# Performance work log

Measured on AMD Instinct MI355X. Metric: run time of the kernel, lower is better.

Reference implementation:

```python
import jax, jax.numpy as jnp
import numpy as np

HEADS = 24
HEAD_DIM = 128
DIM = HEADS * HEAD_DIM  # 3072
EPS = 1e-6


def setup_inputs() -> dict:
    key = jax.random.key(0)
    ks = jax.random.split(key, 10)
    B, S_IMG, S_TXT = 1, 2048, 256
    hidden_states = jax.random.normal(ks[0], (B, S_IMG, DIM), jnp.float32)
    encoder_hidden_states = jax.random.normal(ks[1], (B, S_TXT, DIM), jnp.float32)
    # RoPE tables for image tokens, interleaved pair layout [S_IMG, HEAD_DIM]
    inv = 1.0 / (10000.0 ** (np.arange(0, HEAD_DIM, 2, dtype=np.float32) / HEAD_DIM))
    ang = np.arange(S_IMG, dtype=np.float32)[:, None] * inv[None, :]  # [S, Dh/2]
    ang = np.repeat(ang, 2, axis=-1)  # [S, Dh], pairs (2i, 2i+1) share angle
    rope_cos = jnp.asarray(np.cos(ang), jnp.float32)
    rope_sin = jnp.asarray(np.sin(ang), jnp.float32)
    s = 0.02
    wq = jax.random.normal(ks[2], (DIM, DIM), jnp.float32) * s
    wk = jax.random.normal(ks[3], (DIM, DIM), jnp.float32) * s
    wv = jax.random.normal(ks[4], (DIM, DIM), jnp.float32) * s
    wo = jax.random.normal(ks[5], (DIM, DIM), jnp.float32) * s
    bq = jax.random.normal(ks[6], (DIM,), jnp.float32) * s
    bk = jax.random.normal(ks[7], (DIM,), jnp.float32) * s
    bv = jax.random.normal(ks[8], (DIM,), jnp.float32) * s
    bo = jax.random.normal(ks[9], (DIM,), jnp.float32) * s
    norm_q_w = jnp.ones((HEAD_DIM,), jnp.float32)
    norm_k_w = jnp.ones((HEAD_DIM,), jnp.float32)
    return dict(hidden_states=hidden_states, encoder_hidden_states=encoder_hidden_states,
                rope_cos=rope_cos, rope_sin=rope_sin,
                wq=wq, bq=bq, wk=wk, bk=bk, wv=wv, bv=bv,
                norm_q_w=norm_q_w, norm_k_w=norm_k_w, wo=wo, bo=bo)


def _rmsnorm(x, w):
    var = jnp.mean(jnp.square(x), axis=-1, keepdims=True)
    return x * jax.lax.rsqrt(var + EPS) * w


def _rope(x, cos, sin):
    # x [B,H,S,Dh]; diffusers apply_rotary_emb with use_real_unbind_dim=-1:
    # pairs are interleaved (x[2i], x[2i+1]) -> rotated = stack(-imag, real)
    xr = x[..., 0::2]
    xi = x[..., 1::2]
    x_rot = jnp.stack([-xi, xr], axis=-1).reshape(x.shape)
    return x * cos + x_rot * sin


def reference(hidden_states, encoder_hidden_states, rope_cos, rope_sin,
              wq, bq, wk, bk, wv, bv, norm_q_w, norm_k_w, wo, bo):
    B, s_img, D = hidden_states.shape
    s_txt = encoder_hidden_states.shape[1]
    S = s_img + s_txt
    x = jnp.concatenate([hidden_states, encoder_hidden_states], axis=1)  # [B,S,D]

    def proj(w, b):
        return (x @ w + b).reshape(B, S, HEADS, HEAD_DIM).transpose(0, 2, 1, 3)  # [B,H,S,Dh]

    q = _rmsnorm(proj(wq, bq), norm_q_w)
    k = _rmsnorm(proj(wk, bk), norm_k_w)
    v = proj(wv, bv)
    # RoPE on image tokens only
    q = jnp.concatenate([_rope(q[:, :, :s_img], rope_cos, rope_sin), q[:, :, s_img:]], axis=2)
    k = jnp.concatenate([_rope(k[:, :, :s_img], rope_cos, rope_sin), k[:, :, s_img:]], axis=2)
    scale = 1.0 / jnp.sqrt(jnp.float32(HEAD_DIM))
    scores = jnp.einsum('bhqd,bhkd->bhqk', q, k) * scale
    attn = jax.nn.softmax(scores, axis=-1)
    out = jnp.einsum('bhqk,bhkd->bhqd', attn, v)
    out = out.transpose(0, 2, 1, 3).reshape(B, S, D)
    img = out[:, :s_img] @ wo + bo  # to_out[0]; to_out[1] is Dropout(p=0) -> identity
    txt = out[:, s_img:]            # to_add_out is None in this branch
    return img, txt
```

## Files before the change

kernel.cpp:

```cpp
#include <hip/hip_runtime.h>
#include <cstdint>

typedef __bf16 bf16_t;
typedef bf16_t bf16x8 __attribute__((ext_vector_type(8)));
typedef bf16_t bf16x4 __attribute__((ext_vector_type(4)));
typedef float  floatx4 __attribute__((ext_vector_type(4)));

#define S_ALL 2304
#define SIMG  2048
#define NH    24
#define HD    128
#define DIM   3072
#define NQKV  9216

#define SHIFT2 17.312340490667562f
#define QSCALE 0.12751744f

typedef __attribute__((address_space(1))) void* gp1_t;
typedef __attribute__((address_space(3))) void* lp3_t;

__device__ __forceinline__ void async16(const void* g, void* l) {
    __builtin_amdgcn_global_load_lds((gp1_t)(g), (lp3_t)(l), 16, 0, 0);
}
__device__ __forceinline__ floatx4 mfma_bf16(bf16x8 a, bf16x8 b, floatx4 c) {
    return __builtin_amdgcn_mfma_f32_16x16x32_bf16(a, b, c, 0, 0, 0);
}
__device__ __forceinline__ void barrier_raw() {
    asm volatile("s_barrier" ::: "memory");
}

__global__ __launch_bounds__(256) void k_convert_x(const float* __restrict__ hid,
                                                   const float* __restrict__ enc,
                                                   bf16_t* __restrict__ xb) {
    long i = ((long)blockIdx.x * 256 + threadIdx.x) * 4;
    const long HN = (long)SIMG * DIM;
    float4 f = (i < HN) ? *(const float4*)(hid + i) : *(const float4*)(enc + (i - HN));
    bf16x4 o;
    o[0] = (bf16_t)f.x; o[1] = (bf16_t)f.y; o[2] = (bf16_t)f.z; o[3] = (bf16_t)f.w;
    *(bf16x4*)(xb + i) = o;
}

__global__ __launch_bounds__(256) void k_wT4(const float* __restrict__ wq, const float* __restrict__ wk,
                                             const float* __restrict__ wv, const float* __restrict__ wo,
                                             bf16_t* __restrict__ wTq, bf16_t* __restrict__ woT) {
    __shared__ __align__(16) bf16_t T[64][72];
    int z = blockIdx.z;
    const float* W = (z == 0) ? wq : (z == 1) ? wk : (z == 2) ? wv : wo;
    bf16_t* Wt = (z < 3) ? (wTq + (long)z * DIM * DIM) : woT;
    int r0 = blockIdx.x * 64, c0 = blockIdx.y * 64;
    int tid = threadIdx.x;
    int lr = tid >> 2, lc = (tid & 3) * 16;
    const float* src = W + (long)(r0 + lr) * DIM + c0 + lc;
#pragma unroll
    for (int i = 0; i < 16; i += 4) {
        float4 f = *(const float4*)(src + i);
        T[lr][lc + i + 0] = (bf16_t)f.x;
        T[lr][lc + i + 1] = (bf16_t)f.y;
        T[lr][lc + i + 2] = (bf16_t)f.z;
        T[lr][lc + i + 3] = (bf16_t)f.w;
    }
    __syncthreads();
    bf16x8 a, b;
#pragma unroll
    for (int i = 0; i < 8; i++) a[i] = T[lc + i][lr];
#pragma unroll
    for (int i = 0; i < 8; i++) b[i] = T[lc + 8 + i][lr];
    bf16_t* dst = Wt + (long)(c0 + lr) * DIM + r0 + lc;
    *(bf16x8*)dst = a;
    *(bf16x8*)(dst + 8) = b;
}

__device__ __forceinline__ void gemm_pipe_256x128(const bf16_t* __restrict__ A,
                                                  const bf16_t* __restrict__ Bt,
                                                  long m0, long n0, const int K,
                                                  char* smem, int tid,
                                                  floatx4 acc[4][4]) {
    const int wave = tid >> 6, lane = tid & 63;
    const int quad = lane >> 4, l16 = lane & 15;
    const int wm = (wave >> 1) * 64;
    const int wn = (wave & 1) * 64;
    const int kxor = ((lane & 7) ^ ((lane >> 3) & 7)) * 8;
    const bf16_t* Ag = A + (m0 + wave * 32 + (lane >> 3)) * K + kxor;
    const bf16_t* Bg = Bt + (n0 + wave * 16 + (lane >> 3)) * K + kxor;
    char* Asl = smem + wave * 4096;
    char* Bsl = smem + 98304 + wave * 2048;

    const int NT = K >> 6;

#pragma unroll
    for (int c2 = 0; c2 < 4; ++c2) async16(Ag + (long)c2 * 8 * K,      Asl + c2 * 1024);
#pragma unroll
    for (int c2 = 0; c2 < 2; ++c2) async16(Bg + (long)c2 * 8 * K,      Bsl + c2 * 1024);
#pragma unroll
    for (int c2 = 0; c2 < 4; ++c2) async16(Ag + (long)c2 * 8 * K + 64, Asl + 32768 + c2 * 1024);
#pragma unroll
    for (int c2 = 0; c2 < 2; ++c2) async16(Bg + (long)c2 * 8 * K + 64, Bsl + 16384 + c2 * 1024);
    asm volatile("s_waitcnt vmcnt(6)" ::: "memory");
    barrier_raw();

    int cur = 0;
    for (int kt = 0; kt < NT; ++kt) {
        const bf16_t* As = (const bf16_t*)(smem + cur * 32768);
        const bf16_t* Bs = (const bf16_t*)(smem + 98304 + cur * 16384);
        int nxt = cur + 2; if (nxt >= 3) nxt -= 3;
        char* Asd = Asl + nxt * 32768;
        char* Bsd = Bsl + nxt * 16384;
        const long kg = (long)(kt + 2) * 64;
        const bool issue = (kt < NT - 2);

        bf16x8 af[4], bfr[4];
        {
            int ch = (quad ^ (l16 & 7)) * 8;
#pragma unroll
            for (int i = 0; i < 4; i++) af[i]  = *(const bf16x8*)&As[(wm + i * 16 + l16) * 64 + ch];
#pragma unroll
            for (int j = 0; j < 4; j++) bfr[j] = *(const bf16x8*)&Bs[(wn + j * 16 + l16) * 64 + ch];
        }
        if (issue) {
            async16(Ag + kg,          Asd);
            async16(Ag + 8 * K + kg,  Asd + 1024);
            async16(Bg + kg,          Bsd);
        }
        barrier_raw();
        __builtin_amdgcn_s_setprio(1);
#pragma unroll
        for (int i = 0; i < 4; i++)
#pragma unroll
            for (int j = 0; j < 4; j++) acc[i][j] = mfma_bf16(af[i], bfr[j], acc[i][j]);
        __builtin_amdgcn_s_setprio(0);

        {
            int ch = ((4 + quad) ^ (l16 & 7)) * 8;
#pragma unroll
            for (int i = 0; i < 4; i++) af[i]  = *(const bf16x8*)&As[(wm + i * 16 + l16) * 64 + ch];
#pragma unroll
            for (int j = 0; j < 4; j++) bfr[j] = *(const bf16x8*)&Bs[(wn + j * 16 + l16) * 64 + ch];
        }
        if (issue) {
            async16(Ag + 16 * K + kg, Asd + 2048);
            async16(Ag + 24 * K + kg, Asd + 3072);
            async16(Bg + 8 * K + kg,  Bsd + 1024);
        }
        barrier_raw();
        __builtin_amdgcn_s_setprio(1);
#pragma unroll
        for (int i = 0; i < 4; i++)
#pragma unroll
            for (int j = 0; j < 4; j++) acc[i][j] = mfma_bf16(af[i], bfr[j], acc[i][j]);
        __builtin_amdgcn_s_setprio(0);

        if (issue) asm volatile("s_waitcnt vmcnt(6)" ::: "memory");
        else       asm volatile("s_waitcnt vmcnt(0)" ::: "memory");
        barrier_raw();
        cur += 1; if (cur >= 3) cur -= 3;
    }
}

__global__ __launch_bounds__(512, 2) void k_gemm_qkv(const bf16_t* __restrict__ A,
                                                     const bf16_t* __restrict__ Bt,
                                                     const float* __restrict__ bq_,
                                                     const float* __restrict__ bk_,
                                                     const float* __restrict__ bv_,
                                                     const float* __restrict__ rope_cos,
                                                     const float* __restrict__ rope_sin,
                                                     const float* __restrict__ nqw,
                                                     const float* __restrict__ nkw,
                                                     bf16_t* __restrict__ qo,
                                                     bf16_t* __restrict__ ko,
                                                     bf16_t* __restrict__ vT) {
    __shared__ __align__(16) char smem[147456];
    int tid = threadIdx.x;
    int wave = tid >> 6, lane = tid & 63;
    int quad = lane >> 4, l16 = lane & 15;
    long m0 = (long)blockIdx.y * 256, n0 = (long)blockIdx.x * 128;
    int t = blockIdx.x / 24, h = blockIdx.x % 24;
    int wm = (wave >> 1) * 64, wn = (wave & 1) * 64;

    floatx4 zero = {0.f, 0.f, 0.f, 0.f};
    floatx4 acc[4][4];
#pragma unroll
    for (int i = 0; i < 4; i++)
#pragma unroll
        for (int j = 0; j < 4; j++) acc[i][j] = zero;

    gemm_pipe_256x128(A, Bt, m0, n0, DIM, smem, tid, acc);

    int dcol[4];
#pragma unroll
    for (int j = 0; j < 4; j++) dcol[j] = wn + j * 16 + l16;

    if (t == 2) {
        float bias4[4];
#pragma unroll
        for (int j = 0; j < 4; j++) bias4[j] = bv_[h * HD + dcol[j]];
        char* vbuf = smem;
        int wmi = wave >> 1;
#pragma unroll
        for (int half = 0; half < 2; ++half) {
            if ((wmi >> 1) == half) {
#pragma unroll
                for (int i = 0; i < 4; i++)
#pragma unroll
                    for (int r = 0; r < 4; r++) {
                        int s_l = wm - half * 128 + i * 16 + quad * 4 + r;
#pragma unroll
                        for (int j = 0; j < 4; j++) {
                            int d = dcol[j];
                            int chunk = d * 16 + ((s_l >> 3) ^ (d & 15));
                            *(bf16_t*)(vbuf + chunk * 16 + (s_l & 7) * 2) = (bf16_t)(acc[i][j][r] + bias4[j]);
                        }
                    }
            }
            __syncthreads();
            int d = tid >> 2, sh = tid & 3;
            bf16_t* dstv = vT + (long)h * HD * S_ALL + (long)d * S_ALL + m0 + half * 128 + sh * 32;
#pragma unroll
            for (int k8 = 0; k8 < 4; ++k8) {
                int s8 = sh * 4 + k8;
                bf16x8 frag = *(const bf16x8*)(vbuf + (d * 16 + (s8 ^ (d & 15))) * 16);
                *(bf16x8*)(dstv + k8 * 8) = frag;
            }
            __syncthreads();
        }
    } else {
        float* ssq = (float*)smem;
        const float* bp = t ? bk_ : bq_;
        const float* nw = t ? nkw : nqw;
        float bias4[4], wv4[4];
#pragma unroll
        for (int j = 0; j < 4; j++) {
            bias4[j] = bp[h * HD + dcol[j]];
            wv4[j] = nw[dcol[j]];
        }
        int wnh = wave & 1;
#pragma unroll
        for (int i = 0; i < 4; i++)
#pragma unroll
            for (int r = 0; r < 4; r++) {
                int row = wm + i * 16 + quad * 4 + r;
                float s2 = 0.f;
#pragma unroll
                for (int j = 0; j < 4; j++) {
                    float v = acc[i][j][r] + bias4[j];
                    acc[i][j][r] = v;
                    s2 += v * v;
                }
                s2 += __shfl_xor(s2, 1);
                s2 += __shfl_xor(s2, 2);
                s2 += __shfl_xor(s2, 4);
                s2 += __shfl_xor(s2, 8);
                if (l16 == 0) ssq[row * 2 + wnh] = s2;
            }
        __syncthreads();
        bf16_t* dst = (t ? ko : qo) + (long)h * S_ALL * HD;
        bool do_rope = (m0 < SIMG);
#pragma unroll
        for (int i = 0; i < 4; i++)
#pragma unroll
            for (int r = 0; r < 4; r++) {
                int row = wm + i * 16 + quad * 4 + r;
                int s_abs = (int)m0 + row;
                float tot = ssq[row * 2] + ssq[row * 2 + 1];
                float rms = rsqrtf(tot * (1.0f / 128.0f) + 1e-6f);
                float y[4];
#pragma unroll
                for (int j = 0; j < 4; j++) y[j] = acc[i][j][r] * rms * wv4[j];
                if (do_rope) {
                    const float* cp = rope_cos + (long)s_abs * HD;
                    const float* sp = rope_sin + (long)s_abs * HD;
#pragma unroll
                    for (int j = 0; j < 4; j++) {
                        float c = cp[dcol[j]], sn = sp[dcol[j]];
                        float px = __shfl_xor(y[j], 1);
                        y[j] = y[j] * c + ((l16 & 1) ? px : -px) * sn;
                    }
                }
#pragma unroll
                for (int j = 0; j < 4; j++) {
                    float v = t ? y[j] : y[j] * QSCALE;
                    dst[(long)s_abs * HD + dcol[j]] = (bf16_t)v;
                }
            }
    }
}

__global__ __launch_bounds__(512, 2) void k_gemm_bt(const bf16_t* __restrict__ A,
                                                    const bf16_t* __restrict__ Bt,
                                                    const float* __restrict__ bias,
                                                    bf16_t* __restrict__ Cb, float* __restrict__ Cf,
                                                    int M, int N, int K) {
    __shared__ __align__(16) char smem[147456];
    int tid = threadIdx.x;
    int wave = tid >> 6, lane = tid & 63;
    int quad = lane >> 4, l16 = lane & 15;
    long m0 = (long)blockIdx.y * 256, n0 = (long)blockIdx.x * 128;
    int wm = (wave >> 1) * 64, wn = (wave & 1) * 64;

    floatx4 zero = {0.f, 0.f, 0.f, 0.f};
    floatx4 acc[4][4];
#pragma unroll
    for (int i = 0; i < 4; i++)
#pragma unroll
        for (int j = 0; j < 4; j++) acc[i][j] = zero;

    gemm_pipe_256x128(A, Bt, m0, n0, K, smem, tid, acc);

#pragma unroll
    for (int i = 0; i < 4; i++) {
        long rowb = m0 + wm + i * 16 + quad * 4;
#pragma unroll
        for (int j = 0; j < 4; j++) {
            long col = n0 + wn + j * 16 + l16;
            float bv = bias ? bias[col] : 0.0f;
#pragma unroll
            for (int r = 0; r < 4; r++) {
                float v = acc[i][j][r] + bv;
                long idx = (rowb + r) * N + col;
                if (Cb) Cb[idx] = (bf16_t)v;
                else    Cf[idx] = v;
            }
        }
    }
}

__global__ __launch_bounds__(256, 2) void k_attn(const bf16_t* __restrict__ q,
                                                 const bf16_t* __restrict__ k,
                                                 const bf16_t* __restrict__ vT,
                                                 bf16_t* __restrict__ ao,
                                                 float* __restrict__ out_txt) {
    __shared__ __align__(16) bf16_t Ks[64 * 128];
    __shared__ __align__(16) bf16_t VTs[128 * 64];
    __shared__ __align__(16) bf16_t Ps[4][2][16 * 64];
    int tid = threadIdx.x, wave = tid >> 6, lane = tid & 63;
    int quad = lane >> 4, l16 = lane & 15;
    int h = blockIdx.y;
    int q0 = blockIdx.x * 128 + wave * 32;
    const long hbase = (long)h * S_ALL * HD;
    const char* kgb = (const char*)(k + hbase);
    const char* vgb = (const char*)(vT + hbase);

    int koffB[4], voffB[4], slotB[4];
#pragma unroll
    for (int c2 = 0; c2 < 4; ++c2) {
        int L = (wave * 4 + c2) * 64 + lane;
        slotB[c2] = L;
        int rk = L >> 4, ck = (L & 15) ^ (rk & 15);
        koffB[c2] = rk * 256 + ck * 16;
        int rv = L >> 3, cv = (L & 7) ^ (rv & 7) ^ (((rv >> 3) & 1) << 2);
        voffB[c2] = rv * (S_ALL * 2) + cv * 16;
    }

    bf16x8 qf[2][4];
#pragma unroll
    for (int st = 0; st < 2; ++st) {
        const bf16_t* qp = q + hbase + (long)(q0 + st * 16 + l16) * HD + quad * 8;
#pragma unroll
        for (int ks = 0; ks < 4; ++ks) qf[st][ks] = *(const bf16x8*)(qp + ks * 32);
    }

    floatx4 zero = {0.f, 0.f, 0.f, 0.f};
    floatx4 o0[8], o1[8];
#pragma unroll
    for (int ni = 0; ni < 8; ++ni) { o0[ni] = zero; o1[ni] = zero; }
    floatx4 lac0 = zero, lac1 = zero;

    for (int kb = 0; kb < S_ALL / 64; ++kb) {
        const char* kg = kgb + (long)kb * 16384;
        const char* vg = vgb + kb * 128;
#pragma unroll
        for (int c2 = 0; c2 < 4; ++c2) {
            async16(kg + koffB[c2], (char*)Ks + slotB[c2] * 16);
            async16(vg + voffB[c2], (char*)VTs + slotB[c2] * 16);
        }
        __syncthreads();

        floatx4 s0[4], s1[4];
#pragma unroll
        for (int ni = 0; ni < 4; ++ni) { s0[ni] = zero; s1[ni] = zero; }
#pragma unroll
        for (int ks = 0; ks < 4; ++ks)
#pragma unroll
            for (int ni = 0; ni < 4; ++ni) {
                int slot = (ni * 16 + l16) * 16 + ((ks * 4 + quad) ^ l16);
                bf16x8 kf = *(const bf16x8*)&Ks[slot * 8];
                s0[ni] = mfma_bf16(qf[0][ks], kf, s0[ni]);
                s1[ni] = mfma_bf16(qf[1][ks], kf, s1[ni]);
            }

#pragma unroll
        for (int st = 0; st < 2; ++st) {
#pragma unroll
            for (int ni = 0; ni < 4; ++ni) {
                floatx4 sv = st ? s1[ni] : s0[ni];
                floatx4 p;
#pragma unroll
                for (int j = 0; j < 4; ++j) p[j] = __builtin_amdgcn_exp2f(sv[j] - SHIFT2);
                if (st) lac1 += p; else lac0 += p;
#pragma unroll
                for (int j = 0; j < 4; ++j) {
                    int r = quad * 4 + j;
                    int chunk = ((ni * 16 + l16) >> 3) ^ ((r >> 1) & 7);
                    Ps[wave][st][r * 64 + chunk * 8 + (l16 & 7)] = (bf16_t)p[j];
                }
            }
        }

        bf16x8 pf[2][2];
#pragma unroll
        for (int st = 0; st < 2; ++st)
#pragma unroll
            for (int k2 = 0; k2 < 2; ++k2) {
                int chunk = (k2 * 4 + quad) ^ ((l16 >> 1) & 7);
                pf[st][k2] = *(const bf16x8*)&Ps[wave][st][l16 * 64 + chunk * 8];
            }

#pragma unroll
        for (int k2 = 0; k2 < 2; ++k2)
#pragma unroll
            for (int ni = 0; ni < 8; ++ni) {
                int r = ni * 16 + l16;
                int c = (k2 * 4 + quad) ^ (l16 & 7) ^ (((l16 >> 3) & 1) << 2);
                bf16x8 vf = *(const bf16x8*)&VTs[r * 64 + c * 8];
                o0[ni] = mfma_bf16(pf[0][k2], vf, o0[ni]);
                o1[ni] = mfma_bf16(pf[1][k2], vf, o1[ni]);
            }
        __syncthreads();
    }

#pragma unroll
    for (int off = 1; off < 16; off <<= 1) {
#pragma unroll
        for (int j = 0; j < 4; ++j) {
            lac0[j] += __shfl_xor(lac0[j], off);
            lac1[j] += __shfl_xor(lac1[j], off);
        }
    }

#pragma unroll
    for (int st = 0; st < 2; ++st) {
#pragma unroll
        for (int j = 0; j < 4; ++j) {
            float rl = 1.0f / (st ? lac1[j] : lac0[j]);
            int s_row = q0 + st * 16 + quad * 4 + j;
#pragma unroll
            for (int ni = 0; ni < 8; ++ni) {
                float v = (st ? o1[ni][j] : o0[ni][j]) * rl;
                int col = h * HD + ni * 16 + l16;
                ao[(long)s_row * DIM + col] = (bf16_t)v;
                if (s_row >= SIMG) out_txt[(long)(s_row - SIMG) * DIM + col] = v;
            }
        }
    }
}

extern "C" void kernel_launch(void* const* d_in, const int* in_sizes, int n_in,
                              void* d_out, int out_size, void* d_ws, size_t ws_size,
                              hipStream_t stream) {
    const float* hid = (const float*)d_in[0];
    const float* enc = (const float*)d_in[1];
    const float* rope_cos = (const float*)d_in[2];
    const float* rope_sin = (const float*)d_in[3];
    const float* wq = (const float*)d_in[4];
    const float* bq = (const float*)d_in[5];
    const float* wk = (const float*)d_in[6];
    const float* bk = (const float*)d_in[7];
    const float* wv = (const float*)d_in[8];
    const float* bv = (const float*)d_in[9];
    const float* nqw = (const float*)d_in[10];
    const float* nkw = (const float*)d_in[11];
    const float* wo = (const float*)d_in[12];
    const float* bo = (const float*)d_in[13];
    float* out = (float*)d_out;

    char* ws = (char*)d_ws;
    bf16_t* xb   = (bf16_t*)(ws);
    bf16_t* wTq  = (bf16_t*)(ws + 14155776L);
    bf16_t* woT  = (bf16_t*)(ws + 70778880L);
    bf16_t* qb   = (bf16_t*)(ws + 89653248L);
    bf16_t* kbuf = (bf16_t*)(ws + 103809024L);
    bf16_t* vT   = (bf16_t*)(ws + 117964800L);
    bf16_t* ao   = (bf16_t*)(ws + 132120576L);

    k_convert_x<<<6912, 256, 0, stream>>>(hid, enc, xb);
    k_wT4<<<dim3(48, 48, 4), 256, 0, stream>>>(wq, wk, wv, wo, wTq, woT);
    k_gemm_qkv<<<dim3(72, 9), 512, 0, stream>>>(xb, wTq, bq, bk, bv, rope_cos, rope_sin,
                                                nqw, nkw, qb, kbuf, vT);
    k_attn<<<dim3(18, 24), 256, 0, stream>>>(qb, kbuf, vT, ao, out + (long)SIMG * DIM);
    k_gemm_bt<<<dim3(24, 8), 512, 0, stream>>>(ao, woT, bo, (bf16_t*)nullptr, out, SIMG, DIM, DIM);
}
```

Baseline: 519.4 us.

## Merge GEMM K-halves into one barrier phase and swizzle block order for XCDs

The GEMM main loop now issues all six async global-to-LDS loads up front, reads both K-halves of the A/B fragments from LDS at once, and runs all 32 MFMAs between a single pair of barriers instead of two. This removes one barrier per K-tile at the cost of holding twice the fragment registers. Both GEMM kernels also switch to a 1-D grid with a block-index swizzle ((bid&7)*stride + bid>>3). The swizzle is meant to group neighbouring tiles on the same XCD so they share L2.

```diff
diff --git a/kernel.cpp b/kernel.cpp
--- a/kernel.cpp
+++ b/kernel.cpp
@@ -108,45 +108,38 @@
         const long kg = (long)(kt + 2) * 64;
         const bool issue = (kt < NT - 2);
 
-        bf16x8 af[4], bfr[4];
-        {
-            int ch = (quad ^ (l16 & 7)) * 8;
-#pragma unroll
-            for (int i = 0; i < 4; i++) af[i]  = *(const bf16x8*)&As[(wm + i * 16 + l16) * 64 + ch];
-#pragma unroll
-            for (int j = 0; j < 4; j++) bfr[j] = *(const bf16x8*)&Bs[(wn + j * 16 + l16) * 64 + ch];
-        }
         if (issue) {
             async16(Ag + kg,          Asd);
             async16(Ag + 8 * K + kg,  Asd + 1024);
-            async16(Bg + kg,          Bsd);
-        }
-        barrier_raw();
-        __builtin_amdgcn_s_setprio(1);
-#pragma unroll
-        for (int i = 0; i < 4; i++)
-#pragma unroll
-            for (int j = 0; j < 4; j++) acc[i][j] = mfma_bf16(af[i], bfr[j], acc[i][j]);
-        __builtin_amdgcn_s_setprio(0);
-
-        {
-            int ch = ((4 + quad) ^ (l16 & 7)) * 8;
-#pragma unroll
-            for (int i = 0; i < 4; i++) af[i]  = *(const bf16x8*)&As[(wm + i * 16 + l16) * 64 + ch];
-#pragma unroll
-            for (int j = 0; j < 4; j++) bfr[j] = *(const bf16x8*)&Bs[(wn + j * 16 + l16) * 64 + ch];
-        }
-        if (issue) {
             async16(Ag + 16 * K + kg, Asd + 2048);
             async16(Ag + 24 * K + kg, Asd + 3072);
+            async16(Bg + kg,          Bsd);
             async16(Bg + 8 * K + kg,  Bsd + 1024);
         }
-        barrier_raw();
+
+        bf16x8 af0[4], bf0[4], af1[4], bf1[4];
+        {
+            int ch0 = (quad ^ (l16 & 7)) * 8;
+            int ch1 = ((4 + quad) ^ (l16 & 7)) * 8;
+#pragma unroll
+            for (int i = 0; i < 4; i++) af0[i] = *(const bf16x8*)&As[(wm + i * 16 + l16) * 64 + ch0];
+#pragma unroll
+            for (int j = 0; j < 4; j++) bf0[j] = *(const bf16x8*)&Bs[(wn + j * 16 + l16) * 64 + ch0];
+#pragma unroll
+            for (int i = 0; i < 4; i++) af1[i] = *(const bf16x8*)&As[(wm + i * 16 + l16) * 64 + ch1];
+#pragma unroll
+            for (int j = 0; j < 4; j++) bf1[j] = *(const bf16x8*)&Bs[(wn + j * 16 + l16) * 64 + ch1];
+        }
+
         __builtin_amdgcn_s_setprio(1);
 #pragma unroll
         for (int i = 0; i < 4; i++)
 #pragma unroll
-            for (int j = 0; j < 4; j++) acc[i][j] = mfma_bf16(af[i], bfr[j], acc[i][j]);
+            for (int j = 0; j < 4; j++) acc[i][j] = mfma_bf16(af0[i], bf0[j], acc[i][j]);
+#pragma unroll
+        for (int i = 0; i < 4; i++)
+#pragma unroll
+            for (int j = 0; j < 4; j++) acc[i][j] = mfma_bf16(af1[i], bf1[j], acc[i][j]);
         __builtin_amdgcn_s_setprio(0);
 
         if (issue) asm volatile("s_waitcnt vmcnt(6)" ::: "memory");
@@ -172,8 +165,11 @@
     int tid = threadIdx.x;
     int wave = tid >> 6, lane = tid & 63;
     int quad = lane >> 4, l16 = lane & 15;
-    long m0 = (long)blockIdx.y * 256, n0 = (long)blockIdx.x * 128;
-    int t = blockIdx.x / 24, h = blockIdx.x % 24;
+    int bid = blockIdx.x;
+    int swz = (bid & 7) * 81 + (bid >> 3);
+    int x_n = swz % 72, y_m = swz / 72;
+    long m0 = (long)y_m * 256, n0 = (long)x_n * 128;
+    int t = x_n / 24, h = x_n % 24;
     int wm = (wave >> 1) * 64, wn = (wave & 1) * 64;
 
     floatx4 zero = {0.f, 0.f, 0.f, 0.f};
@@ -293,7 +289,10 @@
     int tid = threadIdx.x;
     int wave = tid >> 6, lane = tid & 63;
     int quad = lane >> 4, l16 = lane & 15;
-    long m0 = (long)blockIdx.y * 256, n0 = (long)blockIdx.x * 128;
+    int bid = blockIdx.x;
+    int swz = (bid & 7) * 24 + (bid >> 3);
+    int x_n = swz % 24, y_m = swz / 24;
+    long m0 = (long)y_m * 256, n0 = (long)x_n * 128;
     int wm = (wave >> 1) * 64, wn = (wave & 1) * 64;
 
     floatx4 zero = {0.f, 0.f, 0.f, 0.f};
@@ -483,8 +482,8 @@
 
     k_convert_x<<<6912, 256, 0, stream>>>(hid, enc, xb);
     k_wT4<<<dim3(48, 48, 4), 256, 0, stream>>>(wq, wk, wv, wo, wTq, woT);
-    k_gemm_qkv<<<dim3(72, 9), 512, 0, stream>>>(xb, wTq, bq, bk, bv, rope_cos, rope_sin,
-                                                nqw, nkw, qb, kbuf, vT);
+    k_gemm_qkv<<<648, 512, 0, stream>>>(xb, wTq, bq, bk, bv, rope_cos, rope_sin,
+                                        nqw, nkw, qb, kbuf, vT);
     k_attn<<<dim3(18, 24), 256, 0, stream>>>(qb, kbuf, vT, ao, out + (long)SIMG * DIM);
-    k_gemm_bt<<<dim3(24, 8), 512, 0, stream>>>(ao, woT, bo, (bf16_t*)nullptr, out, SIMG, DIM, DIM);
-}
+    k_gemm_bt<<<192, 512, 0, stream>>>(ao, woT, bo, (bf16_t*)nullptr, out, SIMG, DIM, DIM);
+}
```

Result: slower. 543.4 us (+4.6%).

## Enlarge GEMM tiles to 256x256 with double-buffered pipeline

Applied to the files above, without the earlier changes.

Switches the QKV and output GEMMs from 256x128 tiles with a three-stage async LDS pipeline to 256x256 tiles with a two-stage double buffer. Each wave now holds an 8x4 accumulator block, and the QKV epilogue is reworked so one block covers two heads. The bigger tiles are meant to raise operand reuse per LDS load and halve the number of blocks. In exchange, register pressure rises, the grid shrinks (324 and 96 blocks), and the shallower prefetch with a full vmcnt(0) wait each step may expose more load latency.

```diff
diff --git a/kernel.cpp b/kernel.cpp
--- a/kernel.cpp
+++ b/kernel.cpp
@@ -70,89 +70,69 @@
     *(bf16x8*)(dst + 8) = b;
 }
 
-__device__ __forceinline__ void gemm_pipe_256x128(const bf16_t* __restrict__ A,
+__device__ __forceinline__ void gemm_pipe_256x256(const bf16_t* __restrict__ A,
                                                   const bf16_t* __restrict__ Bt,
                                                   long m0, long n0, const int K,
                                                   char* smem, int tid,
-                                                  floatx4 acc[4][4]) {
+                                                  floatx4 acc[8][4]) {
     const int wave = tid >> 6, lane = tid & 63;
     const int quad = lane >> 4, l16 = lane & 15;
-    const int wm = (wave >> 1) * 64;
-    const int wn = (wave & 1) * 64;
+    const int wm = (wave >> 2) * 128;
+    const int wn = (wave & 3) * 64;
     const int kxor = ((lane & 7) ^ ((lane >> 3) & 7)) * 8;
     const bf16_t* Ag = A + (m0 + wave * 32 + (lane >> 3)) * K + kxor;
-    const bf16_t* Bg = Bt + (n0 + wave * 16 + (lane >> 3)) * K + kxor;
+    const bf16_t* Bg = Bt + (n0 + wave * 32 + (lane >> 3)) * K + kxor;
     char* Asl = smem + wave * 4096;
-    char* Bsl = smem + 98304 + wave * 2048;
+    char* Bsl = smem + 65536 + wave * 4096;
 
     const int NT = K >> 6;
 
 #pragma unroll
-    for (int c2 = 0; c2 < 4; ++c2) async16(Ag + (long)c2 * 8 * K,      Asl + c2 * 1024);
-#pragma unroll
-    for (int c2 = 0; c2 < 2; ++c2) async16(Bg + (long)c2 * 8 * K,      Bsl + c2 * 1024);
-#pragma unroll
-    for (int c2 = 0; c2 < 4; ++c2) async16(Ag + (long)c2 * 8 * K + 64, Asl + 32768 + c2 * 1024);
-#pragma unroll
-    for (int c2 = 0; c2 < 2; ++c2) async16(Bg + (long)c2 * 8 * K + 64, Bsl + 16384 + c2 * 1024);
-    asm volatile("s_waitcnt vmcnt(6)" ::: "memory");
+    for (int c2 = 0; c2 < 4; ++c2) async16(Ag + (long)c2 * 8 * K, Asl + c2 * 1024);
+#pragma unroll
+    for (int c2 = 0; c2 < 4; ++c2) async16(Bg + (long)c2 * 8 * K, Bsl + c2 * 1024);
+    asm volatile("s_waitcnt vmcnt(0)" ::: "memory");
     barrier_raw();
 
-    int cur = 0;
     for (int kt = 0; kt < NT; ++kt) {
+        const int cur = kt & 1;
         const bf16_t* As = (const bf16_t*)(smem + cur * 32768);
-        const bf16_t* Bs = (const bf16_t*)(smem + 98304 + cur * 16384);
-        int nxt = cur + 2; if (nxt >= 3) nxt -= 3;
-        char* Asd = Asl + nxt * 32768;
-        char* Bsd = Bsl + nxt * 16384;
-        const long kg = (long)(kt + 2) * 64;
-        const bool issue = (kt < NT - 2);
-
-        bf16x8 af[4], bfr[4];
-        {
-            int ch = (quad ^ (l16 & 7)) * 8;
-#pragma unroll
-            for (int i = 0; i < 4; i++) af[i]  = *(const bf16x8*)&As[(wm + i * 16 + l16) * 64 + ch];
+        const bf16_t* Bs = (const bf16_t*)(smem + 65536 + cur * 32768);
+
+        if (kt + 1 < NT) {
+            const long kg = (long)(kt + 1) * 64;
+            char* Asd = Asl + (cur ^ 1) * 32768;
+            char* Bsd = Bsl + (cur ^ 1) * 32768;
+#pragma unroll
+            for (int c2 = 0; c2 < 4; ++c2) async16(Ag + (long)c2 * 8 * K + kg, Asd + c2 * 1024);
+#pragma unroll
+            for (int c2 = 0; c2 < 4; ++c2) async16(Bg + (long)c2 * 8 * K + kg, Bsd + c2 * 1024);
+        }
+
+#pragma unroll
+        for (int ks = 0; ks < 2; ++ks) {
+            const int ch = ((ks * 4 + quad) ^ (l16 & 7)) * 8;
+            bf16x8 bfr[4];
 #pragma unroll
             for (int j = 0; j < 4; j++) bfr[j] = *(const bf16x8*)&Bs[(wn + j * 16 + l16) * 64 + ch];
-        }
-        if (issue) {
-            async16(Ag + kg,          Asd);
-            async16(Ag + 8 * K + kg,  Asd + 1024);
-            async16(Bg + kg,          Bsd);
-        }
+#pragma unroll
+            for (int g = 0; g < 2; ++g) {
+                bf16x8 af[4];
+#pragma unroll
+                for (int i = 0; i < 4; i++)
+                    af[i] = *(const bf16x8*)&As[(wm + (g * 4 + i) * 16 + l16) * 64 + ch];
+                __builtin_amdgcn_s_setprio(1);
+#pragma unroll
+                for (int i = 0; i < 4; i++)
+#pragma unroll
+                    for (int j = 0; j < 4; j++)
+                        acc[g * 4 + i][j] = mfma_bf16(af[i], bfr[j], acc[g * 4 + i][j]);
+                __builtin_amdgcn_s_setprio(0);
+            }
+        }
+
+        asm volatile("s_waitcnt vmcnt(0)" ::: "memory");
         barrier_raw();
-        __builtin_amdgcn_s_setprio(1);
-#pragma unroll
-        for (int i = 0; i < 4; i++)
-#pragma unroll
-            for (int j = 0; j < 4; j++) acc[i][j] = mfma_bf16(af[i], bfr[j], acc[i][j]);
-        __builtin_amdgcn_s_setprio(0);
-
-        {
-            int ch = ((4 + quad) ^ (l16 & 7)) * 8;
-#pragma unroll
-            for (int i = 0; i < 4; i++) af[i]  = *(const bf16x8*)&As[(wm + i * 16 + l16) * 64 + ch];
-#pragma unroll
-            for (int j = 0; j < 4; j++) bfr[j] = *(const bf16x8*)&Bs[(wn + j * 16 + l16) * 64 + ch];
-        }
-        if (issue) {
-            async16(Ag + 16 * K + kg, Asd + 2048);
-            async16(Ag + 24 * K + kg, Asd + 3072);
-            async16(Bg + 8 * K + kg,  Bsd + 1024);
-        }
-        barrier_raw();
-        __builtin_amdgcn_s_setprio(1);
-#pragma unroll
-        for (int i = 0; i < 4; i++)
-#pragma unroll
-            for (int j = 0; j < 4; j++) acc[i][j] = mfma_bf16(af[i], bfr[j], acc[i][j]);
-        __builtin_amdgcn_s_setprio(0);
-
-        if (issue) asm volatile("s_waitcnt vmcnt(6)" ::: "memory");
-        else       asm volatile("s_waitcnt vmcnt(0)" ::: "memory");
-        barrier_raw();
-        cur += 1; if (cur >= 3) cur -= 3;
     }
 }
 
@@ -168,73 +148,79 @@
                                                      bf16_t* __restrict__ qo,
                                                      bf16_t* __restrict__ ko,
                                                      bf16_t* __restrict__ vT) {
-    __shared__ __align__(16) char smem[147456];
+    __shared__ __align__(16) char smem[131072];
     int tid = threadIdx.x;
     int wave = tid >> 6, lane = tid & 63;
     int quad = lane >> 4, l16 = lane & 15;
-    long m0 = (long)blockIdx.y * 256, n0 = (long)blockIdx.x * 128;
-    int t = blockIdx.x / 24, h = blockIdx.x % 24;
-    int wm = (wave >> 1) * 64, wn = (wave & 1) * 64;
+    int x_n = blockIdx.x, y_m = blockIdx.y;
+    long m0 = (long)y_m * 256, n0 = (long)x_n * 256;
+    int t = x_n / 12, hb = (x_n % 12) * 2;
+    int wm = (wave >> 2) * 128, wn = (wave & 3) * 64;
+    int h2w = (wave & 3) >> 1;
+    int halfw = wave & 1;
 
     floatx4 zero = {0.f, 0.f, 0.f, 0.f};
-    floatx4 acc[4][4];
-#pragma unroll
-    for (int i = 0; i < 4; i++)
+    floatx4 acc[8][4];
+#pragma unroll
+    for (int i = 0; i < 8; i++)
 #pragma unroll
         for (int j = 0; j < 4; j++) acc[i][j] = zero;
 
-    gemm_pipe_256x128(A, Bt, m0, n0, DIM, smem, tid, acc);
+    gemm_pipe_256x256(A, Bt, m0, n0, DIM, smem, tid, acc);
 
     int dcol[4];
 #pragma unroll
-    for (int j = 0; j < 4; j++) dcol[j] = wn + j * 16 + l16;
+    for (int j = 0; j < 4; j++) dcol[j] = halfw * 64 + j * 16 + l16;
 
     if (t == 2) {
-        float bias4[4];
-#pragma unroll
-        for (int j = 0; j < 4; j++) bias4[j] = bv_[h * HD + dcol[j]];
         char* vbuf = smem;
-        int wmi = wave >> 1;
-#pragma unroll
-        for (int half = 0; half < 2; ++half) {
-            if ((wmi >> 1) == half) {
-#pragma unroll
-                for (int i = 0; i < 4; i++)
-#pragma unroll
-                    for (int r = 0; r < 4; r++) {
-                        int s_l = wm - half * 128 + i * 16 + quad * 4 + r;
-#pragma unroll
-                        for (int j = 0; j < 4; j++) {
-                            int d = dcol[j];
-                            int chunk = d * 16 + ((s_l >> 3) ^ (d & 15));
-                            *(bf16_t*)(vbuf + chunk * 16 + (s_l & 7) * 2) = (bf16_t)(acc[i][j][r] + bias4[j]);
+#pragma unroll
+        for (int h2 = 0; h2 < 2; ++h2)
+#pragma unroll
+            for (int rh = 0; rh < 2; ++rh) {
+                if ((wave >> 2) == rh && h2w == h2) {
+                    float bias4[4];
+#pragma unroll
+                    for (int j = 0; j < 4; j++) bias4[j] = bv_[(hb + h2) * HD + dcol[j]];
+#pragma unroll
+                    for (int i = 0; i < 8; i++)
+#pragma unroll
+                        for (int r = 0; r < 4; r++) {
+                            int s_l = i * 16 + quad * 4 + r;
+#pragma unroll
+                            for (int j = 0; j < 4; j++) {
+                                int d = dcol[j];
+                                int chunk = d * 16 + ((s_l >> 3) ^ (d & 15));
+                                *(bf16_t*)(vbuf + chunk * 16 + (s_l & 7) * 2) =
+                                    (bf16_t)(acc[i][j][r] + bias4[j]);
+                            }
                         }
-                    }
-            }
-            __syncthreads();
-            int d = tid >> 2, sh = tid & 3;
-            bf16_t* dstv = vT + (long)h * HD * S_ALL + (long)d * S_ALL + m0 + half * 128 + sh * 32;
-#pragma unroll
-            for (int k8 = 0; k8 < 4; ++k8) {
-                int s8 = sh * 4 + k8;
-                bf16x8 frag = *(const bf16x8*)(vbuf + (d * 16 + (s8 ^ (d & 15))) * 16);
-                *(bf16x8*)(dstv + k8 * 8) = frag;
-            }
-            __syncthreads();
-        }
+                }
+                __syncthreads();
+                int d = tid >> 2, sh = tid & 3;
+                bf16_t* dstv = vT + (long)(hb + h2) * HD * S_ALL + (long)d * S_ALL
+                             + m0 + rh * 128 + sh * 32;
+#pragma unroll
+                for (int k8 = 0; k8 < 4; ++k8) {
+                    int s8 = sh * 4 + k8;
+                    bf16x8 frag = *(const bf16x8*)(vbuf + (d * 16 + (s8 ^ (d & 15))) * 16);
+                    *(bf16x8*)(dstv + k8 * 8) = frag;
+                }
+                __syncthreads();
+            }
     } else {
         float* ssq = (float*)smem;
         const float* bp = t ? bk_ : bq_;
         const float* nw = t ? nkw : nqw;
+        int h = hb + h2w;
         float bias4[4], wv4[4];
 #pragma unroll
         for (int j = 0; j < 4; j++) {
             bias4[j] = bp[h * HD + dcol[j]];
             wv4[j] = nw[dcol[j]];
         }
-        int wnh = wave & 1;
-#pragma unroll
-        for (int i = 0; i < 4; i++)
+#pragma unroll
+        for (int i = 0; i < 8; i++)
 #pragma unroll
             for (int r = 0; r < 4; r++) {
                 int row = wm + i * 16 + quad * 4 + r;
@@ -249,18 +235,18 @@
                 s2 += __shfl_xor(s2, 2);
                 s2 += __shfl_xor(s2, 4);
                 s2 += __shfl_xor(s2, 8);
-                if (l16 == 0) ssq[row * 2 + wnh] = s2;
+                if (l16 == 0) ssq[(h2w * 256 + row) * 2 + halfw] = s2;
             }
         __syncthreads();
         bf16_t* dst = (t ? ko : qo) + (long)h * S_ALL * HD;
         bool do_rope = (m0 < SIMG);
 #pragma unroll
-        for (int i = 0; i < 4; i++)
+        for (int i = 0; i < 8; i++)
 #pragma unroll
             for (int r = 0; r < 4; r++) {
                 int row = wm + i * 16 + quad * 4 + r;
                 int s_abs = (int)m0 + row;
-                float tot = ssq[row * 2] + ssq[row * 2 + 1];
+                float tot = ssq[(h2w * 256 + row) * 2] + ssq[(h2w * 256 + row) * 2 + 1];
                 float rms = rsqrtf(tot * (1.0f / 128.0f) + 1e-6f);
                 float y[4];
 #pragma unroll
@@ -289,24 +275,24 @@
                                                     const float* __restrict__ bias,
                                                     bf16_t* __restrict__ Cb, float* __restrict__ Cf,
                                                     int M, int N, int K) {
-    __shared__ __align__(16) char smem[147456];
+    __shared__ __align__(16) char smem[131072];
     int tid = threadIdx.x;
     int wave = tid >> 6, lane = tid & 63;
     int quad = lane >> 4, l16 = lane & 15;
-    long m0 = (long)blockIdx.y * 256, n0 = (long)blockIdx.x * 128;
-    int wm = (wave >> 1) * 64, wn = (wave & 1) * 64;
+    long m0 = (long)blockIdx.y * 256, n0 = (long)blockIdx.x * 256;
+    int wm = (wave >> 2) * 128, wn = (wave & 3) * 64;
 
     floatx4 zero = {0.f, 0.f, 0.f, 0.f};
-    floatx4 acc[4][4];
-#pragma unroll
-    for (int i = 0; i < 4; i++)
+    floatx4 acc[8][4];
+#pragma unroll
+    for (int i = 0; i < 8; i++)
 #pragma unroll
         for (int j = 0; j < 4; j++) acc[i][j] = zero;
 
-    gemm_pipe_256x128(A, Bt, m0, n0, K, smem, tid, acc);
-
-#pragma unroll
-    for (int i = 0; i < 4; i++) {
+    gemm_pipe_256x256(A, Bt, m0, n0, K, smem, tid, acc);
+
+#pragma unroll
+    for (int i = 0; i < 8; i++) {
         long rowb = m0 + wm + i * 16 + quad * 4;
 #pragma unroll
         for (int j = 0; j < 4; j++) {
@@ -483,8 +469,8 @@
 
     k_convert_x<<<6912, 256, 0, stream>>>(hid, enc, xb);
     k_wT4<<<dim3(48, 48, 4), 256, 0, stream>>>(wq, wk, wv, wo, wTq, woT);
-    k_gemm_qkv<<<dim3(72, 9), 512, 0, stream>>>(xb, wTq, bq, bk, bv, rope_cos, rope_sin,
+    k_gemm_qkv<<<dim3(36, 9), 512, 0, stream>>>(xb, wTq, bq, bk, bv, rope_cos, rope_sin,
                                                 nqw, nkw, qb, kbuf, vT);
     k_attn<<<dim3(18, 24), 256, 0, stream>>>(qb, kbuf, vT, ao, out + (long)SIMG * DIM);
-    k_gemm_bt<<<dim3(24, 8), 512, 0, stream>>>(ao, woT, bo, (bf16_t*)nullptr, out, SIMG, DIM, DIM);
-}
+    k_gemm_bt<<<dim3(12, 8), 512, 0, stream>>>(ao, woT, bo, (bf16_t*)nullptr, out, SIMG, DIM, DIM);
+}
```

Measured after the change: 576.3 us. +11.0%, slower.
